# Kernel optimization log

Hardware: AMD Instinct MI355X
Metric: run time of the kernel (lower is better)

The kernel has to match this reference:

```python
import jax, jax.numpy as jnp
import numpy as np

N_NODES = 50000
DEG = 16           # constant out-degree per center node
CUTOFF = 5.0


def setup_inputs() -> dict:
    key = jax.random.key(0)
    k1, k2 = jax.random.split(key)
    # positions scaled so a meaningful fraction of edges exceed the cutoff
    pos = jax.random.normal(k1, (N_NODES, 3), dtype=jnp.float32) * 3.0
    row = jnp.repeat(jnp.arange(N_NODES, dtype=jnp.int32), DEG)      # [E]
    col = jax.random.randint(k2, (N_NODES * DEG,), 0, N_NODES, dtype=jnp.int32)
    edge_index = jnp.stack([row, col], axis=0)                        # [2, E]
    return {"pos": pos, "edge_index": edge_index}


def reference(pos, edge_index):
    """Padded, vectorized DimeNet-style triplet generation.

    Assumes constant degree: edge_index[0] == repeat(arange(N), DEG), so the
    neighbor list of node i is edge_index[1].reshape(N, DEG)[i]. Triplets are
    the [N, DEG, DEG] all-pairs grid; `mask` marks entries that the original
    Python-loop implementation would actually emit (both edges within cutoff,
    j-slot != k-slot).  Masked slots carry 0 for angles/distances.
    """
    num_nodes = pos.shape[0]
    deg = edge_index.shape[1] // num_nodes
    nb = edge_index[1].reshape(num_nodes, deg)          # [N, d] neighbor ids

    R1 = pos[nb] - pos[:, None, :]                      # [N, d, 3] i -> neighbor vectors
    edge_dist = jnp.linalg.norm(R1, axis=-1)            # [N, d]
    valid = edge_dist <= CUTOFF                         # cutoff filter per edge

    diag = jnp.eye(deg, dtype=bool)
    mask = valid[:, :, None] & valid[:, None, :] & ~diag  # [N, d, d]

    # angle(j, i, k) = atan2(|R1_j x R1_k|, R1_j . R1_k)
    dot = jnp.einsum('njc,nkc->njk', R1, R1)            # [N, d, d]
    cross = jnp.cross(R1[:, :, None, :], R1[:, None, :, :])  # [N, d, d, 3]
    cn2 = jnp.sum(cross * cross, axis=-1)
    cross_norm = jnp.sqrt(jnp.where(mask, cn2, 1.0))    # safe sqrt on padded slots
    angles = jnp.where(mask, jnp.arctan2(cross_norm, dot), 0.0)

    # |pos_j - pos_k| = |R1_j - R1_k|
    dvec = R1[:, :, None, :] - R1[:, None, :, :]
    d2 = jnp.sum(dvec * dvec, axis=-1)
    distances_jk = jnp.where(mask, jnp.sqrt(jnp.where(mask & (d2 > 0), d2, 1.0)), 0.0)

    shape3 = (num_nodes, deg, deg)
    id3_i = jnp.broadcast_to(jnp.arange(num_nodes, dtype=jnp.int32)[:, None, None], shape3).reshape(-1)
    id3_j = jnp.broadcast_to(nb[:, :, None], shape3).reshape(-1)
    id3_k = jnp.broadcast_to(nb[:, None, :], shape3).reshape(-1)

    return (id3_i, id3_j, id3_k,
            distances_jk.reshape(-1), angles.reshape(-1), mask.reshape(-1))
```

## Files before the change

### kernel.cpp

```cpp
#include <hip/hip_runtime.h>


#define DEG 16
#define NODES_PER_BLOCK 4
#define CUTOFF_F 5.0f

typedef float f32x4 __attribute__((ext_vector_type(4)));

__device__ __forceinline__ float fast_atan2_pos(float y, float x) {
    const float PI_F   = 3.14159274f;
    const float PIO2_F = 1.57079637f;
    const float ax = fabsf(x);
    const float mn = fminf(ax, y);
    const float mx = fmaxf(ax, y);
    const float a = (mx > 0.0f) ? __fdividef(mn, mx) : 0.0f;
    const float s = a * a;
    float r = fmaf(s, fmaf(s, fmaf(s, fmaf(s, 0.0208351f, -0.085133f),
                                   0.180141f), -0.3302995f), 0.9998660f);
    r *= a;
    if (y > ax)    r = PIO2_F - r;
    if (x < 0.0f)  r = PI_F - r;
    return r;
}

__global__ __launch_bounds__(256) void triplet_kernel(
    const float* __restrict__ pos,
    const int* __restrict__ col_idx,
    float* __restrict__ out,
    int num_nodes, int P)
{
    __shared__ float sx[64], sy[64], sz[64];
    __shared__ float scolf[64];
    __shared__ int   sval[64];

    const int base = blockIdx.x * NODES_PER_BLOCK;
    const int tid = threadIdx.x;

    if (tid < 64) {
        int nl = tid >> 4;
        int slot = tid & 15;
        int node = base + nl;
        if (node < num_nodes) {
            int c = col_idx[node * DEG + slot];
            float px = pos[3 * node], py = pos[3 * node + 1], pz = pos[3 * node + 2];
            float rx = pos[3 * c]     - px;
            float ry = pos[3 * c + 1] - py;
            float rz = pos[3 * c + 2] - pz;
            float d = sqrtf(rx * rx + ry * ry + rz * rz);
            sx[tid] = rx; sy[tid] = ry; sz[tid] = rz;
            scolf[tid] = (float)c;
            sval[tid] = (d <= CUTOFF_F) ? 1 : 0;
        }
    }
    __syncthreads();

    const int w = tid >> 6;
    const int lane = tid & 63;
    const int node = base + w;
    if (node >= num_nodes) return;

    const int ofs = w * DEG;
    const int j = lane >> 2;
    const int k0 = (lane & 3) << 2;

    const float jx = sx[ofs + j], jy = sy[ofs + j], jz = sz[ofs + j];
    const int   jv = sval[ofs + j];
    const float jcolf = scolf[ofs + j];

    f32x4 o_k, o_d, o_a, o_m;

    #pragma unroll
    for (int q = 0; q < 4; ++q) {
        const int k = k0 + q;
        const float kx = sx[ofs + k], ky = sy[ofs + k], kz = sz[ofs + k];
        const int   kv = sval[ofs + k];
        const bool m = (jv != 0) && (kv != 0) && (j != k);

        const float dot = jx * kx + jy * ky + jz * kz;
        const float cx = jy * kz - jz * ky;
        const float cy = jz * kx - jx * kz;
        const float cz = jx * ky - jy * kx;
        const float cn2 = cx * cx + cy * cy + cz * cz;
        const float ang = m ? fast_atan2_pos(sqrtf(cn2), dot) : 0.0f;

        const float dx = jx - kx, dy = jy - ky, dz = jz - kz;
        const float d2 = dx * dx + dy * dy + dz * dz;
        const float dist = m ? sqrtf(d2 > 0.0f ? d2 : 1.0f) : 0.0f;

        o_k[q] = scolf[ofs + k];
        o_d[q] = dist;
        o_a[q] = ang;
        o_m[q] = m ? 1.0f : 0.0f;
    }

    const int idx = node * (DEG * DEG) + lane * 4;
    const float fi = (float)node;
    f32x4 o_i; o_i[0] = fi; o_i[1] = fi; o_i[2] = fi; o_i[3] = fi;
    f32x4 o_j; o_j[0] = jcolf; o_j[1] = jcolf; o_j[2] = jcolf; o_j[3] = jcolf;

    float* o0 = out + idx;
    *reinterpret_cast<f32x4*>(o0)         = o_i;
    *reinterpret_cast<f32x4*>(o0 + P)     = o_j;
    *reinterpret_cast<f32x4*>(o0 + 2 * P) = o_k;
    *reinterpret_cast<f32x4*>(o0 + 3 * P) = o_d;
    *reinterpret_cast<f32x4*>(o0 + 4 * P) = o_a;
    *reinterpret_cast<f32x4*>(o0 + 5 * P) = o_m;
}

extern "C" void kernel_launch(void* const* d_in, const int* in_sizes, int n_in,
                              void* d_out, int out_size, void* d_ws, size_t ws_size,
                              hipStream_t stream) {
    const float* pos = (const float*)d_in[0];
    const int* edge_index = (const int*)d_in[1];

    const int num_nodes = in_sizes[0] / 3;
    const int E = in_sizes[1] / 2;
    const int* col = edge_index + E;

    const int P = num_nodes * (DEG * DEG);
    const int blocks = (num_nodes + NODES_PER_BLOCK - 1) / NODES_PER_BLOCK;

    triplet_kernel<<<blocks, 256, 0, stream>>>(
        pos, col, (float*)d_out, num_nodes, P);
}
```

Measured before the change: 54.69 us.

## Use persistent grid-stride waves with per-wave double-buffered LDS staging

```diff
diff --git a/kernel.cpp b/kernel.cpp
--- a/kernel.cpp
+++ b/kernel.cpp
@@ -2,7 +2,8 @@
 
 
 #define DEG 16
-#define NODES_PER_BLOCK 4
+#define WAVES_PER_BLOCK 4
+#define NBLOCKS 2048
 #define CUTOFF_F 5.0f
 
 typedef float f32x4 __attribute__((ext_vector_type(4)));
@@ -29,82 +30,84 @@
     float* __restrict__ out,
     int num_nodes, int P)
 {
-    __shared__ float sx[64], sy[64], sz[64];
-    __shared__ float scolf[64];
-    __shared__ int   sval[64];
+    __shared__ float sx[2][64], sy[2][64], sz[2][64], scolf[2][64];
+    __shared__ int   sval[2][64];
 
-    const int base = blockIdx.x * NODES_PER_BLOCK;
     const int tid = threadIdx.x;
-
-    if (tid < 64) {
-        int nl = tid >> 4;
-        int slot = tid & 15;
-        int node = base + nl;
-        if (node < num_nodes) {
-            int c = col_idx[node * DEG + slot];
-            float px = pos[3 * node], py = pos[3 * node + 1], pz = pos[3 * node + 2];
-            float rx = pos[3 * c]     - px;
-            float ry = pos[3 * c + 1] - py;
-            float rz = pos[3 * c + 2] - pz;
-            float d = sqrtf(rx * rx + ry * ry + rz * rz);
-            sx[tid] = rx; sy[tid] = ry; sz[tid] = rz;
-            scolf[tid] = (float)c;
-            sval[tid] = (d <= CUTOFF_F) ? 1 : 0;
-        }
-    }
-    __syncthreads();
-
     const int w = tid >> 6;
     const int lane = tid & 63;
-    const int node = base + w;
-    if (node >= num_nodes) return;
+    const int wave_global = blockIdx.x * WAVES_PER_BLOCK + w;
+    const int stride = NBLOCKS * WAVES_PER_BLOCK;
 
-    const int ofs = w * DEG;
+    const int ofs = w << 4;
     const int j = lane >> 2;
     const int k0 = (lane & 3) << 2;
 
-    const float jx = sx[ofs + j], jy = sy[ofs + j], jz = sz[ofs + j];
-    const int   jv = sval[ofs + j];
-    const float jcolf = scolf[ofs + j];
+    int buf = 0;
+    for (int node = wave_global; node < num_nodes; node += stride, buf ^= 1) {
+        const int node_u = __builtin_amdgcn_readfirstlane(node);
 
-    f32x4 o_k, o_d, o_a, o_m;
+        if (lane < DEG) {
+            const int c = col_idx[node_u * DEG + lane];
+            const float px = pos[3 * node_u];
+            const float py = pos[3 * node_u + 1];
+            const float pz = pos[3 * node_u + 2];
+            const float rx = pos[3 * c]     - px;
+            const float ry = pos[3 * c + 1] - py;
+            const float rz = pos[3 * c + 2] - pz;
+            const float d = sqrtf(rx * rx + ry * ry + rz * rz);
+            sx[buf][ofs + lane] = rx;
+            sy[buf][ofs + lane] = ry;
+            sz[buf][ofs + lane] = rz;
+            scolf[buf][ofs + lane] = (float)c;
+            sval[buf][ofs + lane] = (d <= CUTOFF_F) ? 1 : 0;
+        }
+        asm volatile("s_waitcnt lgkmcnt(0)" ::: "memory");
+        __builtin_amdgcn_wave_barrier();
 
-    #pragma unroll
-    for (int q = 0; q < 4; ++q) {
-        const int k = k0 + q;
-        const float kx = sx[ofs + k], ky = sy[ofs + k], kz = sz[ofs + k];
-        const int   kv = sval[ofs + k];
-        const bool m = (jv != 0) && (kv != 0) && (j != k);
+        const float jx = sx[buf][ofs + j], jy = sy[buf][ofs + j], jz = sz[buf][ofs + j];
+        const int   jv = sval[buf][ofs + j];
+        const float jcolf = scolf[buf][ofs + j];
 
-        const float dot = jx * kx + jy * ky + jz * kz;
-        const float cx = jy * kz - jz * ky;
-        const float cy = jz * kx - jx * kz;
-        const float cz = jx * ky - jy * kx;
-        const float cn2 = cx * cx + cy * cy + cz * cz;
-        const float ang = m ? fast_atan2_pos(sqrtf(cn2), dot) : 0.0f;
+        f32x4 o_k, o_d, o_a, o_m;
 
-        const float dx = jx - kx, dy = jy - ky, dz = jz - kz;
-        const float d2 = dx * dx + dy * dy + dz * dz;
-        const float dist = m ? sqrtf(d2 > 0.0f ? d2 : 1.0f) : 0.0f;
+        #pragma unroll
+        for (int q = 0; q < 4; ++q) {
+            const int k = k0 + q;
+            const float kx = sx[buf][ofs + k], ky = sy[buf][ofs + k], kz = sz[buf][ofs + k];
+            const int   kv = sval[buf][ofs + k];
+            const bool m = (jv != 0) && (kv != 0) && (j != k);
 
-        o_k[q] = scolf[ofs + k];
-        o_d[q] = dist;
-        o_a[q] = ang;
-        o_m[q] = m ? 1.0f : 0.0f;
+            const float dot = jx * kx + jy * ky + jz * kz;
+            const float cx = jy * kz - jz * ky;
+            const float cy = jz * kx - jx * kz;
+            const float cz = jx * ky - jy * kx;
+            const float cn2 = cx * cx + cy * cy + cz * cz;
+            const float ang = m ? fast_atan2_pos(sqrtf(cn2), dot) : 0.0f;
+
+            const float dx = jx - kx, dy = jy - ky, dz = jz - kz;
+            const float d2 = dx * dx + dy * dy + dz * dz;
+            const float dist = m ? sqrtf(d2 > 0.0f ? d2 : 1.0f) : 0.0f;
+
+            o_k[q] = scolf[buf][ofs + k];
+            o_d[q] = dist;
+            o_a[q] = ang;
+            o_m[q] = m ? 1.0f : 0.0f;
+        }
+
+        const int idx = node * (DEG * DEG) + lane * 4;
+        const float fi = (float)node;
+        f32x4 o_i; o_i[0] = fi; o_i[1] = fi; o_i[2] = fi; o_i[3] = fi;
+        f32x4 o_j; o_j[0] = jcolf; o_j[1] = jcolf; o_j[2] = jcolf; o_j[3] = jcolf;
+
+        float* o0 = out + idx;
+        *reinterpret_cast<f32x4*>(o0)         = o_i;
+        *reinterpret_cast<f32x4*>(o0 + P)     = o_j;
+        *reinterpret_cast<f32x4*>(o0 + 2 * P) = o_k;
+        *reinterpret_cast<f32x4*>(o0 + 3 * P) = o_d;
+        *reinterpret_cast<f32x4*>(o0 + 4 * P) = o_a;
+        *reinterpret_cast<f32x4*>(o0 + 5 * P) = o_m;
     }
-
-    const int idx = node * (DEG * DEG) + lane * 4;
-    const float fi = (float)node;
-    f32x4 o_i; o_i[0] = fi; o_i[1] = fi; o_i[2] = fi; o_i[3] = fi;
-    f32x4 o_j; o_j[0] = jcolf; o_j[1] = jcolf; o_j[2] = jcolf; o_j[3] = jcolf;
-
-    float* o0 = out + idx;
-    *reinterpret_cast<f32x4*>(o0)         = o_i;
-    *reinterpret_cast<f32x4*>(o0 + P)     = o_j;
-    *reinterpret_cast<f32x4*>(o0 + 2 * P) = o_k;
-    *reinterpret_cast<f32x4*>(o0 + 3 * P) = o_d;
-    *reinterpret_cast<f32x4*>(o0 + 4 * P) = o_a;
-    *reinterpret_cast<f32x4*>(o0 + 5 * P) = o_m;
 }
 
 extern "C" void kernel_launch(void* const* d_in, const int* in_sizes, int n_in,
@@ -118,8 +121,7 @@
     const int* col = edge_index + E;
 
     const int P = num_nodes * (DEG * DEG);
-    const int blocks = (num_nodes + NODES_PER_BLOCK - 1) / NODES_PER_BLOCK;
 
-    triplet_kernel<<<blocks, 256, 0, stream>>>(
+    triplet_kernel<<<NBLOCKS, WAVES_PER_BLOCK * 64, 0, stream>>>(
         pos, col, (float*)d_out, num_nodes, P);
 }
```

New measurement: 68.43 us. 25.1% more time.
